# Optimization experiments

Measured on AMD Instinct MI355X. Metric: run time of the kernel, lower is better.

Reference implementation:

```python
import jax, jax.numpy as jnp
import numpy as np

B, S, D, H = 2, 2048, 1024, 16
DEPTH = D // H  # 64


def setup_inputs() -> dict:
    key = jax.random.key(0)
    ks = jax.random.split(key, 12)
    sc = 0.02
    q = jax.random.normal(ks[0], (B, S, D), jnp.float32)
    k = jax.random.normal(ks[1], (B, S, D), jnp.float32)
    v = jax.random.normal(ks[2], (B, S, D), jnp.float32)
    mask = jax.random.randint(ks[3], (1, 1, S, S), 0, 2, jnp.int32)
    Wq = jax.random.normal(ks[4], (D, D), jnp.float32) * sc
    bq = jnp.zeros((D,), jnp.float32)
    Wk = jax.random.normal(ks[5], (D, D), jnp.float32) * sc
    bk = jnp.zeros((D,), jnp.float32)
    Wv = jax.random.normal(ks[6], (D, DEPTH), jnp.float32) * sc
    bv = jnp.zeros((DEPTH,), jnp.float32)
    Wo = jax.random.normal(ks[7], (DEPTH, D), jnp.float32) * sc
    bo = jnp.zeros((D,), jnp.float32)
    return {"q": q, "k": k, "v": v, "mask": mask,
            "Wq": Wq, "bq": bq, "Wk": Wk, "bk": bk,
            "Wv": Wv, "bv": bv, "Wo": Wo, "bo": bo}


def reference(q, k, v, mask, Wq, bq, Wk, bk, Wv, bv, Wo, bo):
    # project and split heads: [B,S,D] -> [B,H,S,depth]
    qh = (q @ Wq + bq).reshape(B, S, H, DEPTH).transpose(0, 2, 1, 3)
    kh = (k @ Wk + bk).reshape(B, S, H, DEPTH).transpose(0, 2, 1, 3)
    vp = v @ Wv + bv  # [B,S,depth], shared across heads (no per-head split)
    scale = 1.0 / jnp.sqrt(jnp.asarray(DEPTH, jnp.float32))
    logits = jnp.einsum("bhqd,bhkd->bhqk", qh, kh) * scale
    logits = logits + mask.astype(logits.dtype) * (-1e9)
    attn = jax.nn.softmax(logits, axis=-1)  # [B,H,Sq,Sk]
    attn_mean = jnp.mean(attn, axis=1)      # [B,Sq,Sk]
    # mean over heads of (attn_h @ v) == mean(attn) @ v since V is shared
    # (dropout is identity at inference)
    ctx = jnp.einsum("bqk,bkd->bqd", attn_mean, vp)  # [B,S,depth]
    out = ctx @ Wo + bo  # [B,S,D]
    return out, attn_mean
```

## Files before the change

### kernel.cpp

```cpp
#include <hip/hip_runtime.h>
#include <hip/hip_bf16.h>

#define BB 2
#define SS 2048
#define DD 1024
#define HH 16
#define DP 64

typedef __bf16 bf16x8 __attribute__((ext_vector_type(8)));
typedef float f32x4 __attribute__((ext_vector_type(4)));

__device__ __forceinline__ unsigned short f2bf(float f) {
  unsigned u = __float_as_uint(f);
  unsigned r = u + 0x7FFFu + ((u >> 16) & 1u);
  return (unsigned short)(r >> 16);
}

__device__ __forceinline__ bf16x8 load8(const unsigned short* p) {
  return __builtin_bit_cast(bf16x8, *(const uint4*)p);
}

__device__ __forceinline__ f32x4 mfma16(bf16x8 a, bf16x8 b, f32x4 c) {
  return __builtin_amdgcn_mfma_f32_16x16x32_bf16(a, b, c, 0, 0, 0);
}

__global__ __launch_bounds__(256) void imha_prep(
    const float* __restrict__ Wq, const float* __restrict__ Wk,
    const float* __restrict__ Wo, const float* __restrict__ Wv,
    const int* __restrict__ mask,
    unsigned short* __restrict__ wqt, unsigned short* __restrict__ wkt,
    unsigned short* __restrict__ wot, unsigned short* __restrict__ wvt,
    unsigned* __restrict__ mb) {
  const int bx = blockIdx.x, t = threadIdx.x;
  if (bx < 2048) {
    const float* src = (bx < 1024) ? Wq : Wk;
    unsigned short* dst = (bx < 1024) ? wqt : wkt;
    const int tile = bx & 1023;
    const int ty = tile >> 5, tx = tile & 31;
    __shared__ float T[32][33];
    const int r = t >> 3, c4 = (t & 7) * 4;
    const float4 v = *(const float4*)&src[(ty * 32 + r) * 1024 + tx * 32 + c4];
    T[r][c4 + 0] = v.x; T[r][c4 + 1] = v.y; T[r][c4 + 2] = v.z; T[r][c4 + 3] = v.w;
    __syncthreads();
    ushort4 o;
    o.x = f2bf(T[c4 + 0][r]); o.y = f2bf(T[c4 + 1][r]);
    o.z = f2bf(T[c4 + 2][r]); o.w = f2bf(T[c4 + 3][r]);
    *(ushort4*)&dst[(tx * 32 + r) * 1024 + ty * 32 + c4] = o;
  } else if (bx < 2304) {
    const int idx = (bx - 2048) * 256 + t;
    const int n = idx >> 6, k = idx & 63;
    wot[idx] = f2bf(Wo[k * 1024 + n]);
  } else if (bx < 2816) {
    const int widx = (bx - 2304) * 256 + t;
    const int qr = widx >> 6, wd = widx & 63;
    const int* mrow = mask + qr * 2048 + wd * 32;
    unsigned wv = 0;
    #pragma unroll
    for (int j4 = 0; j4 < 8; ++j4) {
      const int4 m4 = *(const int4*)&mrow[j4 * 4];
      wv |= (unsigned)(m4.x & 1) << (j4 * 4);
      wv |= (unsigned)(m4.y & 1) << (j4 * 4 + 1);
      wv |= (unsigned)(m4.z & 1) << (j4 * 4 + 2);
      wv |= (unsigned)(m4.w & 1) << (j4 * 4 + 3);
    }
    mb[widx] = wv;
  } else {
    const int widx = (bx - 2816) * 256 + t;
    const int k = widx >> 6, n = widx & 63;
    wvt[n * 1024 + k] = f2bf(Wv[widx]);
  }
}

__global__ __launch_bounds__(256) void imha_proj(
    const float* __restrict__ X, const unsigned short* __restrict__ Wt,
    const float* __restrict__ bias, unsigned short* __restrict__ dst,
    float preScale) {
  __shared__ unsigned short As[64][40];
  __shared__ unsigned short Bs[128][40];
  const int t = threadIdx.x, l = t & 63, w = t >> 6, lr = l & 15, lg = l >> 4;
  const int m0 = blockIdx.x * 64, n0 = blockIdx.y * 128;
  const int wr = w >> 1, wc = w & 1;
  const f32x4 zf = {0.f, 0.f, 0.f, 0.f};
  f32x4 acc[2][4];
  #pragma unroll
  for (int i = 0; i < 2; ++i)
    #pragma unroll
    for (int j = 0; j < 4; ++j) acc[i][j] = zf;

  for (int kk = 0; kk < 32; ++kk) {
    {
      const int rA = t >> 2, cA = (t & 3) * 8;
      const float4 v0 = *(const float4*)&X[(m0 + rA) * 1024 + kk * 32 + cA];
      const float4 v1 = *(const float4*)&X[(m0 + rA) * 1024 + kk * 32 + cA + 4];
      ushort4 o0, o1;
      o0.x = f2bf(v0.x); o0.y = f2bf(v0.y); o0.z = f2bf(v0.z); o0.w = f2bf(v0.w);
      o1.x = f2bf(v1.x); o1.y = f2bf(v1.y); o1.z = f2bf(v1.z); o1.w = f2bf(v1.w);
      *(ushort4*)&As[rA][cA] = o0;
      *(ushort4*)&As[rA][cA + 4] = o1;
      const int rB = t >> 2, cB = (t & 3) * 8;
      #pragma unroll
      for (int p = 0; p < 2; ++p) {
        const uint4 u = *(const uint4*)&Wt[(n0 + p * 64 + rB) * 1024 + kk * 32 + cB];
        *(uint4*)&Bs[p * 64 + rB][cB] = u;
      }
    }
    __syncthreads();
    bf16x8 a[2], bf[4];
    #pragma unroll
    for (int i = 0; i < 2; ++i) a[i] = load8(&As[wr * 32 + i * 16 + lr][lg * 8]);
    #pragma unroll
    for (int j = 0; j < 4; ++j) bf[j] = load8(&Bs[wc * 64 + j * 16 + lr][lg * 8]);
    #pragma unroll
    for (int i = 0; i < 2; ++i)
      #pragma unroll
      for (int j = 0; j < 4; ++j) acc[i][j] = mfma16(a[i], bf[j], acc[i][j]);
    __syncthreads();
  }
  #pragma unroll
  for (int j = 0; j < 4; ++j) {
    const int gn = n0 + wc * 64 + j * 16 + lr;
    const float bv = bias[gn];
    const int h = gn >> 6, d = gn & 63;
    #pragma unroll
    for (int i = 0; i < 2; ++i) {
      #pragma unroll
      for (int r = 0; r < 4; ++r) {
        const int gm = m0 + wr * 32 + i * 16 + lg * 4 + r;
        const int b = gm >> 11, s = gm & 2047;
        dst[(((b * 16 + h) * 2048 + s) << 6) + d] = f2bf((acc[i][j][r] + bv) * preScale);
      }
    }
  }
}

__global__ __launch_bounds__(256) void imha_vproj_mm(
    const float* __restrict__ V, const unsigned short* __restrict__ wvt,
    float* __restrict__ ctxvp) {
  const int t = threadIdx.x, l = t & 63, w = t >> 6, lr = l & 15, lg = l >> 4;
  const int m0 = blockIdx.x * 64 + w * 16;
  const int k0 = blockIdx.y * 128;
  const f32x4 zf = {0.f, 0.f, 0.f, 0.f};
  f32x4 acc[4];
  #pragma unroll
  for (int j = 0; j < 4; ++j) acc[j] = zf;
  #pragma unroll
  for (int kk = 0; kk < 4; ++kk) {
    const int kb = k0 + kk * 32 + lg * 8;
    const float4 v0 = *(const float4*)&V[(m0 + lr) * 1024 + kb];
    const float4 v1 = *(const float4*)&V[(m0 + lr) * 1024 + kb + 4];
    union { bf16x8 v; unsigned short u[8]; } au;
    au.u[0] = f2bf(v0.x); au.u[1] = f2bf(v0.y); au.u[2] = f2bf(v0.z); au.u[3] = f2bf(v0.w);
    au.u[4] = f2bf(v1.x); au.u[5] = f2bf(v1.y); au.u[6] = f2bf(v1.z); au.u[7] = f2bf(v1.w);
    #pragma unroll
    for (int j = 0; j < 4; ++j) {
      const bf16x8 bfr = load8(&wvt[(j * 16 + lr) * 1024 + kb]);
      acc[j] = mfma16(au.v, bfr, acc[j]);
    }
  }
  #pragma unroll
  for (int j = 0; j < 4; ++j)
    #pragma unroll
    for (int reg = 0; reg < 4; ++reg) {
      const int m = m0 + lg * 4 + reg;
      ctxvp[((size_t)blockIdx.y * 4096 + m) * 64 + j * 16 + lr] = acc[j][reg];
    }
}

__global__ __launch_bounds__(256) void imha_vred(
    const float* __restrict__ ctxvp, const float* __restrict__ bv,
    unsigned short* __restrict__ vpt) {
  __shared__ float T[128][65];
  const int t = threadIdx.x;
  const int m0 = blockIdx.x * 128;
  #pragma unroll
  for (int i = 0; i < 32; ++i) {
    const int e = t + i * 256;
    float s = 0.f;
    #pragma unroll
    for (int p = 0; p < 8; ++p) s += ctxvp[(size_t)p * 262144 + (size_t)m0 * 64 + e];
    T[e >> 6][e & 63] = s;
  }
  __syncthreads();
  const int d = t >> 2, sc = (t & 3) * 32;
  const int b = m0 >> 11, srow = m0 & 2047;
  const float bias = bv[d];
  unsigned short* dst = vpt + ((size_t)b * 64 + d) * 2048 + srow + sc;
  #pragma unroll
  for (int i = 0; i < 32; i += 8) {
    ushort4 o0, o1;
    o0.x = f2bf(T[sc + i + 0][d] + bias); o0.y = f2bf(T[sc + i + 1][d] + bias);
    o0.z = f2bf(T[sc + i + 2][d] + bias); o0.w = f2bf(T[sc + i + 3][d] + bias);
    o1.x = f2bf(T[sc + i + 4][d] + bias); o1.y = f2bf(T[sc + i + 5][d] + bias);
    o1.z = f2bf(T[sc + i + 6][d] + bias); o1.w = f2bf(T[sc + i + 7][d] + bias);
    *(ushort4*)(dst + i) = o0;
    *(ushort4*)(dst + i + 4) = o1;
  }
}

__global__ __launch_bounds__(256, 3) void imha_pass1(
    const unsigned short* __restrict__ qhb, const unsigned short* __restrict__ khb,
    const unsigned* __restrict__ mb, float* __restrict__ lpart) {
  __shared__ unsigned short Kb[2][8192];
  const int t = threadIdx.x, l = t & 63, w = t >> 6, lr = l & 15, lg = l >> 4;
  const int q0 = blockIdx.x * 128, ks = blockIdx.y;
  const int b = blockIdx.z >> 1, hg = blockIdx.z & 1;
  const int k00 = ks * 128;
  const int qw = q0 + w * 32;
  f32x4 aini[2][2][4];
  #pragma unroll
  for (int rf = 0; rf < 2; ++rf)
    #pragma unroll
    for (int reg = 0; reg < 4; ++reg) {
      const int qrow = qw + rf * 16 + lg * 4 + reg;
      const unsigned* mrow = mb + qrow * 64;
      #pragma unroll
      for (int kt = 0; kt < 2; ++kt)
        #pragma unroll
        for (int cf = 0; cf < 4; ++cf) {
          const unsigned word = mrow[(k00 + kt * 64 + cf * 16) >> 5];
          const unsigned bit = (word >> (((cf & 1) << 4) + lr)) & 1u;
          aini[rf][kt][cf][reg] = bit ? -30000.0f : 0.0f;
        }
    }
  const unsigned short* kbase = khb + ((size_t)((b * 16 + hg * 8) * 2048 + k00) << 6);
  uint4 pre[4];
  #pragma unroll
  for (int it = 0; it < 4; ++it)
    pre[it] = *(const uint4*)((const char*)kbase + (it * 256 + t) * 16);
  #pragma unroll
  for (int it = 0; it < 4; ++it) {
    const int off = (it * 256 + t) * 16, row = off >> 7, col = off & 127;
    *(uint4*)((char*)&Kb[0][0] + row * 128 + (col ^ ((row & 7) << 4))) = pre[it];
  }
  __syncthreads();
  #pragma unroll 1
  for (int hh = 0; hh < 8; ++hh) {
    const int h = hg * 8 + hh;
    if (hh < 7) {
      const char* nk = (const char*)(kbase + ((size_t)(hh + 1) << 17));
      #pragma unroll
      for (int it = 0; it < 4; ++it)
        pre[it] = *(const uint4*)(nk + (it * 256 + t) * 16);
    }
    const unsigned short* qb = qhb + ((size_t)((b * 16 + h) * 2048 + qw) << 6);
    bf16x8 aq[2][2];
    #pragma unroll
    for (int rf = 0; rf < 2; ++rf)
      #pragma unroll
      for (int k2 = 0; k2 < 2; ++k2)
        aq[rf][k2] = load8(qb + (((rf * 16 + lr) << 6) + k2 * 32 + lg * 8));
    const char* kl = (const char*)&Kb[hh & 1][0];
    const int sxor = (lr & 7) << 4;
    float lsum[2][4] = {0.f, 0.f, 0.f, 0.f, 0.f, 0.f, 0.f, 0.f};
    #pragma unroll
    for (int kt = 0; kt < 2; ++kt) {
      #pragma unroll
      for (int cf = 0; cf < 4; ++cf) {
        const int row = kt * 64 + cf * 16 + lr;
        const bf16x8 b0 = load8((const unsigned short*)(kl + row * 128 + ((lg * 16) ^ sxor)));
        const bf16x8 b1 = load8((const unsigned short*)(kl + row * 128 + ((64 + lg * 16) ^ sxor)));
        #pragma unroll
        for (int rf = 0; rf < 2; ++rf) {
          f32x4 acc = mfma16(aq[rf][0], b0, aini[rf][kt][cf]);
          acc = mfma16(aq[rf][1], b1, acc);
          #pragma unroll
          for (int reg = 0; reg < 4; ++reg)
            lsum[rf][reg] += __builtin_exp2f(acc[reg]);
        }
      }
    }
    if (hh < 7) {
      #pragma unroll
      for (int it = 0; it < 4; ++it) {
        const int off = (it * 256 + t) * 16, row = off >> 7, col = off & 127;
        *(uint4*)((char*)&Kb[(hh + 1) & 1][0] + row * 128 + (col ^ ((row & 7) << 4))) = pre[it];
      }
      __syncthreads();
    }
    #pragma unroll
    for (int rf = 0; rf < 2; ++rf)
      #pragma unroll
      for (int reg = 0; reg < 4; ++reg) {
        float s = lsum[rf][reg];
        s += __shfl_xor(s, 1, 16); s += __shfl_xor(s, 2, 16);
        s += __shfl_xor(s, 4, 16); s += __shfl_xor(s, 8, 16);
        if (lr == 0)
          lpart[ks * 65536 + (b * 16 + h) * 2048 + qw + rf * 16 + lg * 4 + reg] = s;
      }
  }
}

__global__ __launch_bounds__(256) void imha_linv(
    const float* __restrict__ lpart, float* __restrict__ linv) {
  const int i = blockIdx.x * 256 + threadIdx.x;
  float s = 0.f;
  #pragma unroll
  for (int p = 0; p < 16; ++p) s += lpart[p * 65536 + i];
  linv[i] = 0.0625f / s;
}

__global__ __launch_bounds__(256, 2) void imha_pass2(
    const unsigned short* __restrict__ qhb, const unsigned short* __restrict__ khb,
    const unsigned short* __restrict__ vpt, const unsigned* __restrict__ mb,
    const float* __restrict__ linv, float* __restrict__ attn_out,
    float* __restrict__ ctxp) {
  __shared__ unsigned short Ps[128][136];
  __shared__ unsigned short Kb[2][8192];
  const int t = threadIdx.x, l = t & 63, w = t >> 6, lr = l & 15, lg = l >> 4;
  const int q0 = blockIdx.x * 128, ksb = blockIdx.y, b = blockIdx.z;
  const int k00 = ksb * 128;
  const int qw = q0 + w * 32;
  f32x4 aini[2][2][4];
  #pragma unroll
  for (int rf = 0; rf < 2; ++rf)
    #pragma unroll
    for (int reg = 0; reg < 4; ++reg) {
      const int qrow = qw + rf * 16 + lg * 4 + reg;
      const unsigned* mrow = mb + qrow * 64;
      #pragma unroll
      for (int kt = 0; kt < 2; ++kt)
        #pragma unroll
        for (int cf = 0; cf < 4; ++cf) {
          const unsigned word = mrow[(k00 + kt * 64 + cf * 16) >> 5];
          const unsigned bit = (word >> (((cf & 1) << 4) + lr)) & 1u;
          aini[rf][kt][cf][reg] = bit ? -30000.0f : 0.0f;
        }
    }
  float pm[2][2][4][4];
  #pragma unroll
  for (int a = 0; a < 2; ++a)
    #pragma unroll
    for (int c = 0; c < 2; ++c)
      #pragma unroll
      for (int d2 = 0; d2 < 4; ++d2)
        #pragma unroll
        for (int e = 0; e < 4; ++e) pm[a][c][d2][e] = 0.f;

  const unsigned short* kbase = khb + ((size_t)((b * 16) * 2048 + k00) << 6);
  uint4 pre[4];
  #pragma unroll
  for (int it = 0; it < 4; ++it)
    pre[it] = *(const uint4*)((const char*)kbase + (it * 256 + t) * 16);
  #pragma unroll
  for (int it = 0; it < 4; ++it) {
    const int off = (it * 256 + t) * 16, row = off >> 7, col = off & 127;
    *(uint4*)((char*)&Kb[0][0] + row * 128 + (col ^ ((row & 7) << 4))) = pre[it];
  }
  __syncthreads();
  #pragma unroll 1
  for (int h = 0; h < 16; ++h) {
    if (h < 15) {
      const char* nk = (const char*)(kbase + ((size_t)(h + 1) << 17));
      #pragma unroll
      for (int it = 0; it < 4; ++it)
        pre[it] = *(const uint4*)(nk + (it * 256 + t) * 16);
    }
    const unsigned short* qb = qhb + ((size_t)((b * 16 + h) * 2048 + qw) << 6);
    bf16x8 aq[2][2];
    #pragma unroll
    for (int rf = 0; rf < 2; ++rf)
      #pragma unroll
      for (int k2 = 0; k2 < 2; ++k2)
        aq[rf][k2] = load8(qb + (((rf * 16 + lr) << 6) + k2 * 32 + lg * 8));
    float4 li4[2];
    #pragma unroll
    for (int rf = 0; rf < 2; ++rf)
      li4[rf] = *(const float4*)&linv[(b * 16 + h) * 2048 + qw + rf * 16 + lg * 4];
    const char* kl = (const char*)&Kb[h & 1][0];
    const int sxor = (lr & 7) << 4;
    #pragma unroll
    for (int kt = 0; kt < 2; ++kt) {
      #pragma unroll
      for (int cf = 0; cf < 4; ++cf) {
        const int row = kt * 64 + cf * 16 + lr;
        const bf16x8 b0 = load8((const unsigned short*)(kl + row * 128 + ((lg * 16) ^ sxor)));
        const bf16x8 b1 = load8((const unsigned short*)(kl + row * 128 + ((64 + lg * 16) ^ sxor)));
        #pragma unroll
        for (int rf = 0; rf < 2; ++rf) {
          f32x4 acc = mfma16(aq[rf][0], b0, aini[rf][kt][cf]);
          acc = mfma16(aq[rf][1], b1, acc);
          const float* lip = (const float*)&li4[rf];
          #pragma unroll
          for (int reg = 0; reg < 4; ++reg)
            pm[rf][kt][cf][reg] += __builtin_exp2f(acc[reg]) * lip[reg];
        }
      }
    }
    if (h < 15) {
      #pragma unroll
      for (int it = 0; it < 4; ++it) {
        const int off = (it * 256 + t) * 16, row = off >> 7, col = off & 127;
        *(uint4*)((char*)&Kb[(h + 1) & 1][0] + row * 128 + (col ^ ((row & 7) << 4))) = pre[it];
      }
      __syncthreads();
    }
  }
  #pragma unroll
  for (int rf = 0; rf < 2; ++rf)
    #pragma unroll
    for (int kt = 0; kt < 2; ++kt)
      #pragma unroll
      for (int cf = 0; cf < 4; ++cf)
        #pragma unroll
        for (int reg = 0; reg < 4; ++reg) {
          const int qrow = qw + rf * 16 + lg * 4 + reg;
          const int col = k00 + kt * 64 + cf * 16 + lr;
          const float p = pm[rf][kt][cf][reg];
          attn_out[((size_t)(b * 2048 + qrow) << 11) + col] = p;
          Ps[w * 32 + rf * 16 + lg * 4 + reg][kt * 64 + cf * 16 + lr] = f2bf(p);
        }
  const f32x4 zf = {0.f, 0.f, 0.f, 0.f};
  f32x4 ctx[2][4];
  #pragma unroll
  for (int rf = 0; rf < 2; ++rf)
    #pragma unroll
    for (int dcf = 0; dcf < 4; ++dcf) ctx[rf][dcf] = zf;
  #pragma unroll
  for (int k2 = 0; k2 < 4; ++k2) {
    bf16x8 ap[2];
    #pragma unroll
    for (int rf = 0; rf < 2; ++rf)
      ap[rf] = load8(&Ps[w * 32 + rf * 16 + lr][k2 * 32 + lg * 8]);
    #pragma unroll
    for (int dcf = 0; dcf < 4; ++dcf) {
      const bf16x8 bvf = load8(vpt + ((size_t)(b * 64 + dcf * 16 + lr)) * 2048 + k00 + k2 * 32 + lg * 8);
      #pragma unroll
      for (int rf = 0; rf < 2; ++rf) ctx[rf][dcf] = mfma16(ap[rf], bvf, ctx[rf][dcf]);
    }
  }
  #pragma unroll
  for (int rf = 0; rf < 2; ++rf)
    #pragma unroll
    for (int dcf = 0; dcf < 4; ++dcf)
      #pragma unroll
      for (int reg = 0; reg < 4; ++reg) {
        const int m = b * 2048 + qw + rf * 16 + lg * 4 + reg;
        ctxp[((size_t)(ksb * 4096 + m) << 6) + dcf * 16 + lr] = ctx[rf][dcf][reg];
      }
}

__global__ __launch_bounds__(256) void imha_ctxred(
    const float* __restrict__ ctxp, unsigned short* __restrict__ ctxr) {
  const int i4 = (blockIdx.x * 256 + threadIdx.x) * 4;
  float4 s = {0.f, 0.f, 0.f, 0.f};
  #pragma unroll
  for (int p = 0; p < 16; ++p) {
    const float4 v = *(const float4*)&ctxp[(size_t)p * 262144 + i4];
    s.x += v.x; s.y += v.y; s.z += v.z; s.w += v.w;
  }
  ushort4 o;
  o.x = f2bf(s.x); o.y = f2bf(s.y); o.z = f2bf(s.z); o.w = f2bf(s.w);
  *(ushort4*)&ctxr[i4] = o;
}

__global__ __launch_bounds__(256) void imha_outproj(
    const unsigned short* __restrict__ ctxr, const unsigned short* __restrict__ wot,
    const float* __restrict__ bo, float* __restrict__ out) {
  __shared__ unsigned short As[128][72];
  __shared__ unsigned short Bs[128][72];
  const int t = threadIdx.x, l = t & 63, w = t >> 6, lr = l & 15, lg = l >> 4;
  const int m0 = blockIdx.x * 128, n0 = blockIdx.y * 128;
  const int wr = w >> 1, wc = w & 1;
  {
    const int r = t >> 1, cs = (t & 1) * 32;
    #pragma unroll
    for (int i = 0; i < 4; ++i)
      *(uint4*)&As[r][cs + i * 8] = *(const uint4*)&ctxr[(m0 + r) * 64 + cs + i * 8];
    #pragma unroll
    for (int i = 0; i < 4; ++i)
      *(uint4*)&Bs[r][cs + i * 8] = *(const uint4*)&wot[(n0 + r) * 64 + cs + i * 8];
  }
  __syncthreads();
  const f32x4 zf = {0.f, 0.f, 0.f, 0.f};
  f32x4 acc[4][4];
  #pragma unroll
  for (int i = 0; i < 4; ++i)
    #pragma unroll
    for (int j = 0; j < 4; ++j) acc[i][j] = zf;
  #pragma unroll
  for (int k2 = 0; k2 < 2; ++k2) {
    bf16x8 a[4], bb[4];
    #pragma unroll
    for (int i = 0; i < 4; ++i) a[i] = load8(&As[wr * 64 + i * 16 + lr][k2 * 32 + lg * 8]);
    #pragma unroll
    for (int i = 0; i < 4; ++i) bb[i] = load8(&Bs[wc * 64 + i * 16 + lr][k2 * 32 + lg * 8]);
    #pragma unroll
    for (int i = 0; i < 4; ++i)
      #pragma unroll
      for (int j = 0; j < 4; ++j) acc[i][j] = mfma16(a[i], bb[j], acc[i][j]);
  }
  #pragma unroll
  for (int j = 0; j < 4; ++j) {
    const int gn = n0 + wc * 64 + j * 16 + lr;
    const float bv = bo[gn];
    #pragma unroll
    for (int i = 0; i < 4; ++i) {
      #pragma unroll
      for (int r = 0; r < 4; ++r) {
        const int gm = m0 + wr * 64 + i * 16 + lg * 4 + r;
        out[((size_t)gm << 10) + gn] = acc[i][j][r] + bv;
      }
    }
  }
}

extern "C" void kernel_launch(void* const* d_in, const int* in_sizes, int n_in,
                              void* d_out, int out_size, void* d_ws, size_t ws_size,
                              hipStream_t stream) {
  const float* q  = (const float*)d_in[0];
  const float* k  = (const float*)d_in[1];
  const float* v  = (const float*)d_in[2];
  const int*  mask = (const int*)d_in[3];
  const float* Wq = (const float*)d_in[4];
  const float* bq = (const float*)d_in[5];
  const float* Wk = (const float*)d_in[6];
  const float* bk = (const float*)d_in[7];
  const float* Wv = (const float*)d_in[8];
  const float* bv = (const float*)d_in[9];
  const float* Wo = (const float*)d_in[10];
  const float* bo = (const float*)d_in[11];

  char* ws = (char*)d_ws;
  unsigned short* wqt  = (unsigned short*)(ws + 0);
  unsigned short* wkt  = (unsigned short*)(ws + 2097152);
  unsigned short* wot  = (unsigned short*)(ws + 4194304);
  unsigned*       mb   = (unsigned*)      (ws + 4325376);
  unsigned short* qhb  = (unsigned short*)(ws + 4849664);
  unsigned short* khb  = (unsigned short*)(ws + 13238272);
  unsigned short* vpt  = (unsigned short*)(ws + 21626880);
  float*          linv = (float*)         (ws + 22151168);
  float*          ctxp = (float*)         (ws + 22413312);
  unsigned short* ctxr = (unsigned short*)(ws + 39190528);
  unsigned short* wvt  = (unsigned short*)(ws + 22413312);
  float*          ctxvp= (float*)         (ws + 22413312 + 131072);
  float*          lpart= (float*)         (ws + 22413312);

  float* out  = (float*)d_out;
  float* attn = out + (size_t)BB * SS * DD;

  const float qScale = 0.125f * 1.44269504088896340736f;

  imha_prep<<<3072, 256, 0, stream>>>(Wq, Wk, Wo, Wv, mask, wqt, wkt, wot, wvt, mb);
  imha_vproj_mm<<<dim3(64, 8), 256, 0, stream>>>(v, wvt, ctxvp);
  imha_vred<<<32, 256, 0, stream>>>(ctxvp, bv, vpt);
  imha_proj<<<dim3(64, 8), 256, 0, stream>>>(q, wqt, bq, qhb, qScale);
  imha_proj<<<dim3(64, 8), 256, 0, stream>>>(k, wkt, bk, khb, 1.0f);
  imha_pass1<<<dim3(16, 16, 4), 256, 0, stream>>>(qhb, khb, mb, lpart);
  imha_linv<<<256, 256, 0, stream>>>(lpart, linv);
  imha_pass2<<<dim3(16, 16, 2), 256, 0, stream>>>(qhb, khb, vpt, mb, linv, attn, ctxp);
  imha_ctxred<<<256, 256, 0, stream>>>(ctxp, ctxr);
  imha_outproj<<<dim3(32, 8), 256, 0, stream>>>(ctxr, wot, bo, out);
}
```

Before: 241.5 us.

## Restructure softmax-denominator pass to loop over keys per head, swizzle block order

Pass1 now gives each block one (batch, head, 128-query) tile and loops over all 16 key tiles, accumulating the row sums in registers. This replaces the old split over key slices and head groups, so per-slice partial-sum writes and repeated Q reloads go away, and mask words are loaded per key tile. Partial sums are stored per lane, 16 per row, and linv reduces them with vector loads. Both pass1 and pass2 use a 1D grid with an XCD-style block swizzle and raise wave priority around the MFMA loop. Pass1 now launches fewer, longer blocks, which could hurt load balance.

```diff
diff --git a/kernel.cpp b/kernel.cpp
--- a/kernel.cpp
+++ b/kernel.cpp
@@ -199,30 +199,21 @@
 
 __global__ __launch_bounds__(256, 3) void imha_pass1(
     const unsigned short* __restrict__ qhb, const unsigned short* __restrict__ khb,
-    const unsigned* __restrict__ mb, float* __restrict__ lpart) {
+    const unsigned* __restrict__ mb, float* __restrict__ lpart16) {
   __shared__ unsigned short Kb[2][8192];
   const int t = threadIdx.x, l = t & 63, w = t >> 6, lr = l & 15, lg = l >> 4;
-  const int q0 = blockIdx.x * 128, ks = blockIdx.y;
-  const int b = blockIdx.z >> 1, hg = blockIdx.z & 1;
-  const int k00 = ks * 128;
+  const int orig = blockIdx.x;
+  const int swz = (orig & 7) * 64 + (orig >> 3);
+  const int q0 = (swz & 15) * 128, bh = swz >> 4;
   const int qw = q0 + w * 32;
-  f32x4 aini[2][2][4];
+  const unsigned short* qb = qhb + ((size_t)(bh * 2048 + qw) << 6);
+  bf16x8 aq[2][2];
   #pragma unroll
   for (int rf = 0; rf < 2; ++rf)
     #pragma unroll
-    for (int reg = 0; reg < 4; ++reg) {
-      const int qrow = qw + rf * 16 + lg * 4 + reg;
-      const unsigned* mrow = mb + qrow * 64;
-      #pragma unroll
-      for (int kt = 0; kt < 2; ++kt)
-        #pragma unroll
-        for (int cf = 0; cf < 4; ++cf) {
-          const unsigned word = mrow[(k00 + kt * 64 + cf * 16) >> 5];
-          const unsigned bit = (word >> (((cf & 1) << 4) + lr)) & 1u;
-          aini[rf][kt][cf][reg] = bit ? -30000.0f : 0.0f;
-        }
-    }
-  const unsigned short* kbase = khb + ((size_t)((b * 16 + hg * 8) * 2048 + k00) << 6);
+    for (int k2 = 0; k2 < 2; ++k2)
+      aq[rf][k2] = load8(qb + (((rf * 16 + lr) << 6) + k2 * 32 + lg * 8));
+  const unsigned short* kbase = khb + ((size_t)bh << 17);
   uint4 pre[4];
   #pragma unroll
   for (int it = 0; it < 4; ++it)
@@ -233,69 +224,76 @@
     *(uint4*)((char*)&Kb[0][0] + row * 128 + (col ^ ((row & 7) << 4))) = pre[it];
   }
   __syncthreads();
+  float lsum[2][4] = {0.f, 0.f, 0.f, 0.f, 0.f, 0.f, 0.f, 0.f};
   #pragma unroll 1
-  for (int hh = 0; hh < 8; ++hh) {
-    const int h = hg * 8 + hh;
-    if (hh < 7) {
-      const char* nk = (const char*)(kbase + ((size_t)(hh + 1) << 17));
+  for (int kt = 0; kt < 16; ++kt) {
+    if (kt < 15) {
+      const char* nk = (const char*)kbase + (kt + 1) * 16384;
       #pragma unroll
       for (int it = 0; it < 4; ++it)
         pre[it] = *(const uint4*)(nk + (it * 256 + t) * 16);
     }
-    const unsigned short* qb = qhb + ((size_t)((b * 16 + h) * 2048 + qw) << 6);
-    bf16x8 aq[2][2];
+    uint4 mw[2][4];
     #pragma unroll
     for (int rf = 0; rf < 2; ++rf)
       #pragma unroll
-      for (int k2 = 0; k2 < 2; ++k2)
-        aq[rf][k2] = load8(qb + (((rf * 16 + lr) << 6) + k2 * 32 + lg * 8));
-    const char* kl = (const char*)&Kb[hh & 1][0];
+      for (int reg = 0; reg < 4; ++reg) {
+        const int qrow = qw + rf * 16 + lg * 4 + reg;
+        mw[rf][reg] = *(const uint4*)&mb[qrow * 64 + kt * 4];
+      }
+    const char* kl = (const char*)&Kb[kt & 1][0];
     const int sxor = (lr & 7) << 4;
-    float lsum[2][4] = {0.f, 0.f, 0.f, 0.f, 0.f, 0.f, 0.f, 0.f};
-    #pragma unroll
-    for (int kt = 0; kt < 2; ++kt) {
-      #pragma unroll
-      for (int cf = 0; cf < 4; ++cf) {
-        const int row = kt * 64 + cf * 16 + lr;
-        const bf16x8 b0 = load8((const unsigned short*)(kl + row * 128 + ((lg * 16) ^ sxor)));
-        const bf16x8 b1 = load8((const unsigned short*)(kl + row * 128 + ((64 + lg * 16) ^ sxor)));
+    __builtin_amdgcn_s_setprio(1);
+    #pragma unroll
+    for (int cf = 0; cf < 8; ++cf) {
+      const int row = cf * 16 + lr;
+      const bf16x8 b0 = load8((const unsigned short*)(kl + row * 128 + ((lg * 16) ^ sxor)));
+      const bf16x8 b1 = load8((const unsigned short*)(kl + row * 128 + ((64 + lg * 16) ^ sxor)));
+      #pragma unroll
+      for (int rf = 0; rf < 2; ++rf) {
+        f32x4 aini;
         #pragma unroll
-        for (int rf = 0; rf < 2; ++rf) {
-          f32x4 acc = mfma16(aq[rf][0], b0, aini[rf][kt][cf]);
-          acc = mfma16(aq[rf][1], b1, acc);
-          #pragma unroll
-          for (int reg = 0; reg < 4; ++reg)
-            lsum[rf][reg] += __builtin_exp2f(acc[reg]);
+        for (int reg = 0; reg < 4; ++reg) {
+          const unsigned word = ((const unsigned*)&mw[rf][reg])[cf >> 1];
+          const unsigned bit = (word >> (((cf & 1) << 4) + lr)) & 1u;
+          aini[reg] = bit ? -30000.0f : 0.0f;
         }
-      }
-    }
-    if (hh < 7) {
+        f32x4 acc = mfma16(aq[rf][0], b0, aini);
+        acc = mfma16(aq[rf][1], b1, acc);
+        #pragma unroll
+        for (int reg = 0; reg < 4; ++reg)
+          lsum[rf][reg] += __builtin_exp2f(acc[reg]);
+      }
+    }
+    __builtin_amdgcn_s_setprio(0);
+    if (kt < 15) {
       #pragma unroll
       for (int it = 0; it < 4; ++it) {
         const int off = (it * 256 + t) * 16, row = off >> 7, col = off & 127;
-        *(uint4*)((char*)&Kb[(hh + 1) & 1][0] + row * 128 + (col ^ ((row & 7) << 4))) = pre[it];
+        *(uint4*)((char*)&Kb[(kt + 1) & 1][0] + row * 128 + (col ^ ((row & 7) << 4))) = pre[it];
       }
       __syncthreads();
     }
-    #pragma unroll
-    for (int rf = 0; rf < 2; ++rf)
-      #pragma unroll
-      for (int reg = 0; reg < 4; ++reg) {
-        float s = lsum[rf][reg];
-        s += __shfl_xor(s, 1, 16); s += __shfl_xor(s, 2, 16);
-        s += __shfl_xor(s, 4, 16); s += __shfl_xor(s, 8, 16);
-        if (lr == 0)
-          lpart[ks * 65536 + (b * 16 + h) * 2048 + qw + rf * 16 + lg * 4 + reg] = s;
-      }
-  }
+  }
+  #pragma unroll
+  for (int rf = 0; rf < 2; ++rf)
+    #pragma unroll
+    for (int reg = 0; reg < 4; ++reg) {
+      const int qrow = bh * 2048 + qw + rf * 16 + lg * 4 + reg;
+      lpart16[(qrow << 4) + lr] = lsum[rf][reg];
+    }
 }
 
 __global__ __launch_bounds__(256) void imha_linv(
-    const float* __restrict__ lpart, float* __restrict__ linv) {
+    const float* __restrict__ lpart16, float* __restrict__ linv) {
   const int i = blockIdx.x * 256 + threadIdx.x;
+  const float4* p = (const float4*)&lpart16[i << 4];
   float s = 0.f;
   #pragma unroll
-  for (int p = 0; p < 16; ++p) s += lpart[p * 65536 + i];
+  for (int j = 0; j < 4; ++j) {
+    const float4 v = p[j];
+    s += v.x + v.y + v.z + v.w;
+  }
   linv[i] = 0.0625f / s;
 }
 
@@ -307,7 +305,9 @@
   __shared__ unsigned short Ps[128][136];
   __shared__ unsigned short Kb[2][8192];
   const int t = threadIdx.x, l = t & 63, w = t >> 6, lr = l & 15, lg = l >> 4;
-  const int q0 = blockIdx.x * 128, ksb = blockIdx.y, b = blockIdx.z;
+  const int orig = blockIdx.x;
+  const int swz = (orig & 7) * 64 + (orig >> 3);
+  const int q0 = (swz & 15) * 128, ksb = (swz >> 4) & 15, b = swz >> 8;
   const int k00 = ksb * 128;
   const int qw = q0 + w * 32;
   f32x4 aini[2][2][4];
@@ -368,6 +368,7 @@
       li4[rf] = *(const float4*)&linv[(b * 16 + h) * 2048 + qw + rf * 16 + lg * 4];
     const char* kl = (const char*)&Kb[h & 1][0];
     const int sxor = (lr & 7) << 4;
+    __builtin_amdgcn_s_setprio(1);
     #pragma unroll
     for (int kt = 0; kt < 2; ++kt) {
       #pragma unroll
@@ -386,6 +387,7 @@
         }
       }
     }
+    __builtin_amdgcn_s_setprio(0);
     if (h < 15) {
       #pragma unroll
       for (int it = 0; it < 4; ++it) {
@@ -533,7 +535,7 @@
   unsigned short* ctxr = (unsigned short*)(ws + 39190528);
   unsigned short* wvt  = (unsigned short*)(ws + 22413312);
   float*          ctxvp= (float*)         (ws + 22413312 + 131072);
-  float*          lpart= (float*)         (ws + 22413312);
+  float*          lpart16 = (float*)      (ws + 22413312);
 
   float* out  = (float*)d_out;
   float* attn = out + (size_t)BB * SS * DD;
@@ -545,9 +547,9 @@
   imha_vred<<<32, 256, 0, stream>>>(ctxvp, bv, vpt);
   imha_proj<<<dim3(64, 8), 256, 0, stream>>>(q, wqt, bq, qhb, qScale);
   imha_proj<<<dim3(64, 8), 256, 0, stream>>>(k, wkt, bk, khb, 1.0f);
-  imha_pass1<<<dim3(16, 16, 4), 256, 0, stream>>>(qhb, khb, mb, lpart);
-  imha_linv<<<256, 256, 0, stream>>>(lpart, linv);
-  imha_pass2<<<dim3(16, 16, 2), 256, 0, stream>>>(qhb, khb, vpt, mb, linv, attn, ctxp);
+  imha_pass1<<<512, 256, 0, stream>>>(qhb, khb, mb, lpart16);
+  imha_linv<<<256, 256, 0, stream>>>(lpart16, linv);
+  imha_pass2<<<512, 256, 0, stream>>>(qhb, khb, vpt, mb, linv, attn, ctxp);
   imha_ctxred<<<256, 256, 0, stream>>>(ctxp, ctxr);
   imha_outproj<<<dim3(32, 8), 256, 0, stream>>>(ctxr, wot, bo, out);
 }
```

New measurement: 221.0 us. 8.5% less time.
